# Performance work log

Hardware: AMD Instinct MI355X
Metric: run time of the kernel (lower is better)

Reference implementation:

```python
import jax, jax.numpy as jnp
import numpy as np

B, V, S, H = 16384, 16, 64, 512


def setup_inputs() -> dict:
    key = jax.random.key(0)
    kx, kw, kb, kws, kbs = jax.random.split(key, 5)
    x = jax.random.normal(kx, (B, V, S), dtype=jnp.float32)
    # per-variable linear layers: weight [V, S, H], bias [V, H]
    W = jax.random.normal(kw, (V, S, H), dtype=jnp.float32) * (1.0 / np.sqrt(S))
    b = jax.random.normal(kb, (V, H), dtype=jnp.float32) * 0.01
    # variable selection linear: hidden -> V
    W_sel = jax.random.normal(kws, (H, V), dtype=jnp.float32) * (1.0 / np.sqrt(H))
    b_sel = jax.random.normal(kbs, (V,), dtype=jnp.float32) * 0.01
    return {"x": x, "W": W, "b": b, "W_sel": W_sel, "b_sel": b_sel}


def reference(x, W, b, W_sel, b_sel):
    # per-variable linears: [B, V, H]
    transformed = jnp.einsum('bvs,vsh->bvh', x, W) + b  # grouped small GEMMs
    # torch stacks to [B, H, V]; mean over variable axis -> [B, H]
    flat = transformed.mean(axis=1)
    # softmax-gated selection weights [B, V] (dropout is identity in eval)
    weights = jax.nn.softmax(flat @ W_sel + b_sel, axis=-1)
    # weighted sum over variables -> [B, H]
    out = jnp.einsum('bvh,bv->bh', transformed, weights)
    return out
```

## Files before the change

### kernel.cpp

```cpp
#include <hip/hip_runtime.h>
#include <hip/hip_bf16.h>
#include <stdint.h>

#define B_ROWS 16384
#define VDIM   16
#define SDIM   64
#define HDIM   512
#define KDIM   1024
#define KP     1056

#define ASTR     1064
#define G_PLOG   68096
#define G_LDS    (68096 + 8704)

#define CSTR     296
#define BUFU16   (64 * CSTR)
#define GEMM_LDS (2 * BUFU16 * 2)

using bf16x8 = __attribute__((ext_vector_type(8))) __bf16;
using u16x8  = __attribute__((ext_vector_type(8))) unsigned short;
using u16x4  = __attribute__((ext_vector_type(4))) unsigned short;
using f32x4  = __attribute__((ext_vector_type(4))) float;

__device__ __forceinline__ unsigned short f2bf(float f) {
  unsigned int u = __builtin_bit_cast(unsigned int, f);
  u = (u + 0x7FFFu + ((u >> 16) & 1u)) >> 16;
  return (unsigned short)u;
}
__device__ __forceinline__ float bf2f(unsigned short s) {
  return __builtin_bit_cast(float, (unsigned int)s << 16);
}

__global__ __launch_bounds__(256) void k0_prep(
    const float* __restrict__ W, const float* __restrict__ bias,
    const float* __restrict__ Wsel, const float* __restrict__ bsel,
    unsigned short* __restrict__ Bt, unsigned short* __restrict__ WcombT,
    float* __restrict__ bcomb) {
  __shared__ float bm[HDIM];
  __shared__ float part[16][17];
  __shared__ unsigned short tile[32][264];
  const int t = threadIdx.x;
  if (blockIdx.x < 66) {
    const int k0 = (blockIdx.x >> 1) * 32;
    const int n  = ((blockIdx.x & 1) << 8) + t;
    #pragma unroll 8
    for (int kk = 0; kk < 32; ++kk) {
      const int k = k0 + kk;
      float val;
      if (k < KDIM)            val = W[(size_t)k * HDIM + n];
      else if (k < KDIM + 16)  val = bias[(size_t)(k - KDIM) * HDIM + n];
      else                     val = 0.f;
      tile[kk][t] = f2bf(val);
    }
    __syncthreads();
    unsigned short* dst = Bt + (size_t)n * KP + k0;
    #pragma unroll
    for (int seg = 0; seg < 4; ++seg) {
      unsigned short o[8];
      #pragma unroll
      for (int jj = 0; jj < 8; ++jj) o[jj] = tile[seg * 8 + jj][t];
      *(u16x8*)(dst + seg * 8) = *(const u16x8*)o;
    }
    return;
  }
  const int bid = blockIdx.x - 66;
  if (bid < 256) {
    const int wave = t >> 6, lane = t & 63;
    const int k = bid * 4 + wave;
    const float* wr = W + (size_t)k * HDIM;
    float s[16];
    #pragma unroll
    for (int v = 0; v < 16; ++v) s[v] = 0.f;
    #pragma unroll
    for (int j = 0; j < 8; ++j) {
      const int h = lane + 64 * j;
      const float a = wr[h];
      const float4* wl = (const float4*)(Wsel + h * 16);
      const float4 q0 = wl[0], q1 = wl[1], q2 = wl[2], q3 = wl[3];
      s[0]  = fmaf(a, q0.x, s[0]);  s[1]  = fmaf(a, q0.y, s[1]);
      s[2]  = fmaf(a, q0.z, s[2]);  s[3]  = fmaf(a, q0.w, s[3]);
      s[4]  = fmaf(a, q1.x, s[4]);  s[5]  = fmaf(a, q1.y, s[5]);
      s[6]  = fmaf(a, q1.z, s[6]);  s[7]  = fmaf(a, q1.w, s[7]);
      s[8]  = fmaf(a, q2.x, s[8]);  s[9]  = fmaf(a, q2.y, s[9]);
      s[10] = fmaf(a, q2.z, s[10]); s[11] = fmaf(a, q2.w, s[11]);
      s[12] = fmaf(a, q3.x, s[12]); s[13] = fmaf(a, q3.y, s[13]);
      s[14] = fmaf(a, q3.z, s[14]); s[15] = fmaf(a, q3.w, s[15]);
    }
    #pragma unroll
    for (int off = 32; off > 0; off >>= 1) {
      #pragma unroll
      for (int v = 0; v < 16; ++v) s[v] += __shfl_xor(s[v], off, 64);
    }
    float mine = 0.f;
    #pragma unroll
    for (int v = 0; v < 16; ++v) mine = (lane == v) ? s[v] : mine;
    if (lane < 16) WcombT[lane * KDIM + k] = f2bf(mine * (1.f / 16.f));
  } else {
    for (int h = t; h < HDIM; h += 256) {
      float s = 0.f;
      #pragma unroll
      for (int v = 0; v < VDIM; ++v) s += bias[v * HDIM + h];
      bm[h] = s * (1.f / 16.f);
    }
    __syncthreads();
    int v = t & 15, sl = t >> 4;
    float s = 0.f;
    for (int h = sl * 32; h < sl * 32 + 32; ++h) s = fmaf(bm[h], Wsel[h * VDIM + v], s);
    part[sl][v] = s;
    __syncthreads();
    if (t < 16) {
      float s2 = bsel[t];
      #pragma unroll
      for (int i = 0; i < 16; ++i) s2 += part[i][t];
      bcomb[t] = s2;
    }
  }
}

__global__ __launch_bounds__(512, 4) void k1_gate(
    const float* __restrict__ x, const unsigned short* __restrict__ WcombT,
    const float* __restrict__ bcomb, float* __restrict__ wgate) {
  extern __shared__ unsigned short As[];
  float* plog = (float*)((char*)As + G_PLOG);

  const int t = threadIdx.x;
  const int rowb = blockIdx.x * 32;
  const int wave = t >> 6, lane = t & 63;
  const int mlane = lane & 15, quad = lane >> 4;

  {
    const int srow = t >> 4;
    const int sc = (t & 15) * 8;
    const float* xr = x + (size_t)(rowb + srow) * KDIM + sc;
    unsigned short* aw = As + srow * ASTR + sc;
    #pragma unroll
    for (int i = 0; i < 8; ++i) {
      const float4 a0 = *(const float4*)(xr + i * 128);
      const float4 a1 = *(const float4*)(xr + i * 128 + 4);
      u16x8 u;
      u[0] = f2bf(a0.x); u[1] = f2bf(a0.y); u[2] = f2bf(a0.z); u[3] = f2bf(a0.w);
      u[4] = f2bf(a1.x); u[5] = f2bf(a1.y); u[6] = f2bf(a1.z); u[7] = f2bf(a1.w);
      *(u16x8*)(aw + i * 128) = u;
    }
  }
  __syncthreads();

  {
    const int kh = wave >> 1, rg = wave & 1;
    const unsigned short* al = As + (rg * 16 + mlane) * ASTR + kh * 256 + quad * 8;
    const unsigned short* bl = WcombT + mlane * KDIM + kh * 256 + quad * 8;
    f32x4 acc = {0.f, 0.f, 0.f, 0.f};
    #pragma unroll
    for (int kt = 0; kt < 8; ++kt) {
      bf16x8 a = *(const bf16x8*)al; al += 32;
      bf16x8 b = *(const bf16x8*)bl; bl += 32;
      acc = __builtin_amdgcn_mfma_f32_16x16x32_bf16(a, b, acc, 0, 0, 0);
    }
    float* pl = plog + ((size_t)((kh * 2 + rg) * 16 + quad * 4) * 17 + mlane);
    #pragma unroll
    for (int r = 0; r < 4; ++r) pl[r * 17] = acc[r];
  }
  __syncthreads();

  if (t < 32) {
    const int rg = t >> 4, rr = t & 15;
    float l[16];
    float mx = -1e30f;
    #pragma unroll
    for (int v = 0; v < 16; ++v) {
      float s = bcomb[v];
      #pragma unroll
      for (int kq = 0; kq < 4; ++kq)
        s += plog[((size_t)((kq * 2 + rg) * 16 + rr)) * 17 + v];
      l[v] = s;
      mx = fmaxf(mx, s);
    }
    float s = 0.f;
    #pragma unroll
    for (int v = 0; v < 16; ++v) { l[v] = __expf(l[v] - mx); s += l[v]; }
    const float inv = 1.f / s;
    float* wo = wgate + (size_t)(rowb + t) * 16;
    #pragma unroll
    for (int q = 0; q < 4; ++q) {
      f32x4 o = {l[4*q] * inv, l[4*q+1] * inv, l[4*q+2] * inv, l[4*q+3] * inv};
      *(f32x4*)(wo + 4 * q) = o;
    }
  }
}

__global__ __launch_bounds__(512, 2) void k2_gemm(
    const float* __restrict__ x, const float* __restrict__ wgate,
    const unsigned short* __restrict__ Bt, float* __restrict__ C) {
  extern __shared__ unsigned short As[];
  const int t = threadIdx.x;
  const int rowb = blockIdx.x * 64;
  const int wave = t >> 6, lane = t & 63;
  const int mlane = lane & 15, quad = lane >> 4;

  const int srow = t >> 3;
  const int sk   = (t & 7) * 32;
  const float* xrow = x + (size_t)(rowb + srow) * KDIM + sk;
  const float* wrow = wgate + (size_t)(rowb + srow) * 16;
  const int vsub = (t & 7) >> 1;
  const float w0 = wrow[vsub], w1 = wrow[4 + vsub],
              w2 = wrow[8 + vsub], w3 = wrow[12 + vsub];

  unsigned short* myA0 = As + srow * CSTR + sk;

  f32x4 xr[8];
  #pragma unroll
  for (int i = 0; i < 8; ++i) xr[i] = *(const f32x4*)(xrow + i * 4);
  {
    #pragma unroll
    for (int s = 0; s < 4; ++s) {
      const f32x4 a = xr[2 * s], b2 = xr[2 * s + 1];
      u16x8 o;
      o[0] = f2bf(w0 * a[0]);  o[1] = f2bf(w0 * a[1]);
      o[2] = f2bf(w0 * a[2]);  o[3] = f2bf(w0 * a[3]);
      o[4] = f2bf(w0 * b2[0]); o[5] = f2bf(w0 * b2[1]);
      o[6] = f2bf(w0 * b2[2]); o[7] = f2bf(w0 * b2[3]);
      *(u16x8*)(myA0 + s * 8) = o;
    }
  }
  #pragma unroll
  for (int i = 0; i < 8; ++i) xr[i] = *(const f32x4*)(xrow + 256 + i * 4);

  const int colb = wave * 64;
  const unsigned short* bp[4];
  #pragma unroll
  for (int j = 0; j < 4; ++j)
    bp[j] = Bt + (size_t)(colb + j * 16 + mlane) * KP + quad * 8;
  bf16x8 bv0[4], bv1[4];
  #pragma unroll
  for (int j = 0; j < 4; ++j) {
    bv0[j] = *(const bf16x8*)(bp[j]);
    bv1[j] = *(const bf16x8*)(bp[j] + 32);
    bp[j] += 64;
  }

  __syncthreads();

  f32x4 acc[4][4];
  const f32x4 z = {0.f, 0.f, 0.f, 0.f};
  #pragma unroll
  for (int i = 0; i < 4; ++i)
    #pragma unroll
    for (int j = 0; j < 4; ++j) acc[i][j] = z;

  int ktg = 0;
  #pragma unroll 1
  for (int c = 0; c < 5; ++c) {
    const unsigned short* buf = As + (c & 1) * BUFU16;
    const int nkt = (c < 4) ? 8 : 1;
    #pragma unroll 1
    for (int kt = 0; kt < nkt; ++kt) {
      bf16x8 bnext[4];
      if (ktg < 31) {
        #pragma unroll
        for (int j = 0; j < 4; ++j) { bnext[j] = *(const bf16x8*)bp[j]; bp[j] += 32; }
      }
      bf16x8 av[4];
      #pragma unroll
      for (int i = 0; i < 4; ++i)
        av[i] = *(const bf16x8*)(buf + (i * 16 + mlane) * CSTR + kt * 32 + quad * 8);
      #pragma unroll
      for (int i = 0; i < 4; ++i)
        #pragma unroll
        for (int j = 0; j < 4; ++j)
          acc[i][j] = __builtin_amdgcn_mfma_f32_16x16x32_bf16(av[i], bv0[j], acc[i][j], 0, 0, 0);
      #pragma unroll
      for (int j = 0; j < 4; ++j) { bv0[j] = bv1[j]; bv1[j] = bnext[j]; }
      ++ktg;
    }
    if (c < 3) {
      unsigned short* dst = As + ((c + 1) & 1) * BUFU16 + srow * CSTR + sk;
      const float ws = (c == 0) ? w1 : (c == 1) ? w2 : w3;
      #pragma unroll
      for (int s = 0; s < 4; ++s) {
        const f32x4 a = xr[2 * s], b2 = xr[2 * s + 1];
        u16x8 o;
        o[0] = f2bf(ws * a[0]);  o[1] = f2bf(ws * a[1]);
        o[2] = f2bf(ws * a[2]);  o[3] = f2bf(ws * a[3]);
        o[4] = f2bf(ws * b2[0]); o[5] = f2bf(ws * b2[1]);
        o[6] = f2bf(ws * b2[2]); o[7] = f2bf(ws * b2[3]);
        *(u16x8*)(dst + s * 8) = o;
      }
      if (c < 2) {
        #pragma unroll
        for (int i = 0; i < 8; ++i)
          xr[i] = *(const f32x4*)(xrow + (c + 2) * 256 + i * 4);
      }
      __syncthreads();
    } else if (c == 3) {
      const int j4 = (t & 7) * 4;
      u16x4 o;
      if (j4 < 16) {
        const f32x4 wv = *(const f32x4*)(wgate + (size_t)(rowb + srow) * 16 + j4);
        o[0] = f2bf(wv[0]); o[1] = f2bf(wv[1]); o[2] = f2bf(wv[2]); o[3] = f2bf(wv[3]);
      } else {
        o[0] = 0; o[1] = 0; o[2] = 0; o[3] = 0;
      }
      *(u16x4*)(As + srow * CSTR + j4) = o;
      __syncthreads();
    }
  }

  #pragma unroll
  for (int i = 0; i < 4; ++i)
    #pragma unroll
    for (int j = 0; j < 4; ++j)
      #pragma unroll
      for (int r = 0; r < 4; ++r) {
        const size_t row = (size_t)rowb + i * 16 + quad * 4 + r;
        const int col = colb + j * 16 + mlane;
        __builtin_nontemporal_store(acc[i][j][r], &C[row * HDIM + col]);
      }
}

extern "C" void kernel_launch(void* const* d_in, const int* in_sizes, int n_in,
                              void* d_out, int out_size, void* d_ws, size_t ws_size,
                              hipStream_t stream) {
  const float* x    = (const float*)d_in[0];
  const float* W    = (const float*)d_in[1];
  const float* bias = (const float*)d_in[2];
  const float* Wsel = (const float*)d_in[3];
  const float* bsel = (const float*)d_in[4];
  float* out = (float*)d_out;

  char* ws = (char*)d_ws;
  unsigned short* Bt     = (unsigned short*)(ws);
  unsigned short* WcombT = (unsigned short*)(ws + 1081344);
  float*          bcomb  = (float*)(ws + 1114112);
  float*          wgate  = (float*)(ws + 1114368);

  static int lds_set = 0;
  if (!lds_set) {
    hipFuncSetAttribute((const void*)k1_gate,
                        hipFuncAttributeMaxDynamicSharedMemorySize, G_LDS);
    hipFuncSetAttribute((const void*)k2_gemm,
                        hipFuncAttributeMaxDynamicSharedMemorySize, GEMM_LDS);
    lds_set = 1;
  }

  k0_prep<<<323, 256, 0, stream>>>(W, bias, Wsel, bsel, Bt, WcombT, bcomb);
  k1_gate<<<512, 512, G_LDS, stream>>>(x, WcombT, bcomb, wgate);
  k2_gemm<<<256, 512, GEMM_LDS, stream>>>(x, wgate, Bt, out);
}
```

Before: 161.1 us.

## Deepen B-operand prefetch to four stages and fully unroll GEMM K loop

```diff
diff --git a/kernel.cpp b/kernel.cpp
--- a/kernel.cpp
+++ b/kernel.cpp
@@ -205,12 +205,11 @@
   const float w0 = wrow[vsub], w1 = wrow[4 + vsub],
               w2 = wrow[8 + vsub], w3 = wrow[12 + vsub];
 
-  unsigned short* myA0 = As + srow * CSTR + sk;
-
   f32x4 xr[8];
   #pragma unroll
   for (int i = 0; i < 8; ++i) xr[i] = *(const f32x4*)(xrow + i * 4);
   {
+    unsigned short* dst = As + srow * CSTR + sk;
     #pragma unroll
     for (int s = 0; s < 4; ++s) {
       const f32x4 a = xr[2 * s], b2 = xr[2 * s + 1];
@@ -219,7 +218,7 @@
       o[2] = f2bf(w0 * a[2]);  o[3] = f2bf(w0 * a[3]);
       o[4] = f2bf(w0 * b2[0]); o[5] = f2bf(w0 * b2[1]);
       o[6] = f2bf(w0 * b2[2]); o[7] = f2bf(w0 * b2[3]);
-      *(u16x8*)(myA0 + s * 8) = o;
+      *(u16x8*)(dst + s * 8) = o;
     }
   }
   #pragma unroll
@@ -230,13 +229,14 @@
   #pragma unroll
   for (int j = 0; j < 4; ++j)
     bp[j] = Bt + (size_t)(colb + j * 16 + mlane) * KP + quad * 8;
-  bf16x8 bv0[4], bv1[4];
-  #pragma unroll
-  for (int j = 0; j < 4; ++j) {
-    bv0[j] = *(const bf16x8*)(bp[j]);
-    bv1[j] = *(const bf16x8*)(bp[j] + 32);
-    bp[j] += 64;
-  }
+  bf16x8 bvs[4][4];
+  #pragma unroll
+  for (int d = 0; d < 4; ++d)
+    #pragma unroll
+    for (int j = 0; j < 4; ++j)
+      bvs[d][j] = *(const bf16x8*)(bp[j] + d * 32);
+  #pragma unroll
+  for (int j = 0; j < 4; ++j) bp[j] += 128;
 
   __syncthreads();
 
@@ -247,34 +247,11 @@
     #pragma unroll
     for (int j = 0; j < 4; ++j) acc[i][j] = z;
 
-  int ktg = 0;
-  #pragma unroll 1
-  for (int c = 0; c < 5; ++c) {
-    const unsigned short* buf = As + (c & 1) * BUFU16;
-    const int nkt = (c < 4) ? 8 : 1;
-    #pragma unroll 1
-    for (int kt = 0; kt < nkt; ++kt) {
-      bf16x8 bnext[4];
-      if (ktg < 31) {
-        #pragma unroll
-        for (int j = 0; j < 4; ++j) { bnext[j] = *(const bf16x8*)bp[j]; bp[j] += 32; }
-      }
-      bf16x8 av[4];
-      #pragma unroll
-      for (int i = 0; i < 4; ++i)
-        av[i] = *(const bf16x8*)(buf + (i * 16 + mlane) * CSTR + kt * 32 + quad * 8);
-      #pragma unroll
-      for (int i = 0; i < 4; ++i)
-        #pragma unroll
-        for (int j = 0; j < 4; ++j)
-          acc[i][j] = __builtin_amdgcn_mfma_f32_16x16x32_bf16(av[i], bv0[j], acc[i][j], 0, 0, 0);
-      #pragma unroll
-      for (int j = 0; j < 4; ++j) { bv0[j] = bv1[j]; bv1[j] = bnext[j]; }
-      ++ktg;
-    }
+  #pragma unroll
+  for (int c = 0; c < 4; ++c) {
     if (c < 3) {
+      const float ws = (c == 0) ? w1 : (c == 1) ? w2 : w3;
       unsigned short* dst = As + ((c + 1) & 1) * BUFU16 + srow * CSTR + sk;
-      const float ws = (c == 0) ? w1 : (c == 1) ? w2 : w3;
       #pragma unroll
       for (int s = 0; s < 4; ++s) {
         const f32x4 a = xr[2 * s], b2 = xr[2 * s + 1];
@@ -290,8 +267,7 @@
         for (int i = 0; i < 8; ++i)
           xr[i] = *(const f32x4*)(xrow + (c + 2) * 256 + i * 4);
       }
-      __syncthreads();
-    } else if (c == 3) {
+    } else {
       const int j4 = (t & 7) * 4;
       u16x4 o;
       if (j4 < 16) {
@@ -301,8 +277,42 @@
         o[0] = 0; o[1] = 0; o[2] = 0; o[3] = 0;
       }
       *(u16x4*)(As + srow * CSTR + j4) = o;
-      __syncthreads();
-    }
+    }
+
+    const unsigned short* buf = As + (c & 1) * BUFU16;
+    #pragma unroll
+    for (int kt = 0; kt < 8; ++kt) {
+      const int ktg = c * 8 + kt;
+      bf16x8 cur[4];
+      #pragma unroll
+      for (int j = 0; j < 4; ++j) cur[j] = bvs[kt & 3][j];
+      if (ktg + 4 <= 32) {
+        #pragma unroll
+        for (int j = 0; j < 4; ++j) { bvs[kt & 3][j] = *(const bf16x8*)bp[j]; bp[j] += 32; }
+      }
+      bf16x8 av[4];
+      #pragma unroll
+      for (int i = 0; i < 4; ++i)
+        av[i] = *(const bf16x8*)(buf + (i * 16 + mlane) * CSTR + kt * 32 + quad * 8);
+      #pragma unroll
+      for (int i = 0; i < 4; ++i)
+        #pragma unroll
+        for (int j = 0; j < 4; ++j)
+          acc[i][j] = __builtin_amdgcn_mfma_f32_16x16x32_bf16(av[i], cur[j], acc[i][j], 0, 0, 0);
+    }
+    __syncthreads();
+  }
+
+  {
+    bf16x8 av[4];
+    #pragma unroll
+    for (int i = 0; i < 4; ++i)
+      av[i] = *(const bf16x8*)(As + (i * 16 + mlane) * CSTR + quad * 8);
+    #pragma unroll
+    for (int i = 0; i < 4; ++i)
+      #pragma unroll
+      for (int j = 0; j < 4; ++j)
+        acc[i][j] = __builtin_amdgcn_mfma_f32_16x16x32_bf16(av[i], bvs[0][j], acc[i][j], 0, 0, 0);
   }
 
   #pragma unroll
```

New measurement: 158.4 us. No clear change (-1.7%).
